# Kernel tuning notes

Hardware: AMD Instinct MI355X
Metric: run time of the kernel (lower is better)

## Reference

```python
import jax, jax.numpy as jnp
import numpy as np

PATCH = 16
TOP_K = 5
EPS = 1e-12


def l2_normalize(x, axis):
    sq = jnp.sum(x * x, axis=axis, keepdims=True)
    return x * jax.lax.rsqrt(jnp.maximum(sq, EPS))


def patch_embed(imgs, conv_w, conv_b):
    # imgs: (P, 3, 32, 32) -> (P, n_patches=4, D=768)
    y = jax.lax.conv_general_dilated(
        imgs, conv_w, window_strides=(PATCH, PATCH), padding='VALID',
        dimension_numbers=('NCHW', 'OIHW', 'NCHW'))  # (P, D, 2, 2)
    y = y + conv_b[None, :, None, None]
    P, D = y.shape[0], y.shape[1]
    return y.reshape(P, D, -1).transpose(0, 2, 1)  # (P, 4, D)


def setup_inputs() -> dict:
    key = jax.random.key(0)
    k1, k2, k3, k4 = jax.random.split(key, 4)
    B, N, D = 256, 196, 768
    P = 32  # pool_size
    x_embed = jax.random.normal(k1, (B, N, D), dtype=jnp.float32)
    # uniform(-1, 1) init as in the torch module
    prompt = jax.random.uniform(k2, (P, 3, 32, 32), dtype=jnp.float32, minval=-1.0, maxval=1.0)
    prompt_key = jax.random.uniform(k3, (P, D), dtype=jnp.float32, minval=-1.0, maxval=1.0)
    conv_w = jax.random.normal(k4, (D, 3, PATCH, PATCH), dtype=jnp.float32) * 0.02
    conv_b = jnp.zeros((D,), dtype=jnp.float32)
    return {'x_embed': x_embed, 'prompt': prompt, 'prompt_key': prompt_key,
            'conv_w': conv_w, 'conv_b': conv_b}


def reference(x_embed, prompt, prompt_key, conv_w, conv_b):
    B = x_embed.shape[0]
    prompt_embed = patch_embed(prompt, conv_w, conv_b)      # (P, 4, D)

    x_embed_mean = jnp.mean(x_embed, axis=1)                # (B, D), embedding_key='mean'
    prompt_norm = l2_normalize(prompt_key, axis=1)          # (P, D)
    x_embed_norm = l2_normalize(x_embed_mean, axis=1)       # (B, D)
    similarity = x_embed_norm @ prompt_norm.T               # (B, P)

    _, idx = jax.lax.top_k(similarity, TOP_K)               # (B, top_k)

    batched_prompt_embed = prompt_embed[idx]                # (B, top_k, 4, D)
    Bq, K, L, D = batched_prompt_embed.shape
    batched_prompt_embed = batched_prompt_embed.reshape(Bq, K * L, D)

    batched_key_norm = prompt_norm[idx]                     # (B, top_k, D)
    reduce_sim = jnp.sum(batched_key_norm * x_embed_norm[:, None, :]) / B

    prompted_embedding = jnp.concatenate([batched_prompt_embed, x_embed], axis=1)
    return prompted_embedding, reduce_sim, similarity, idx
```

## Files before the change

kernel.cpp:

```cpp
#include <hip/hip_runtime.h>

typedef unsigned short u16;
typedef unsigned int u32;

#define BB 256
#define NN 196
#define DD 768
#define PP 32
#define TOPK 5
#define NROW 216

#define OUT0_ELTS (BB * NROW * DD)
#define RS_OFF    OUT0_ELTS
#define SIM_OFF   (OUT0_ELTS + 1)
#define IDX_OFF   (OUT0_ELTS + 1 + BB * PP)

#define WS_PNORM  0
#define WS_PEMB   98304
#define WS_IDX    491520

__global__ __launch_bounds__(256) void k_prep(const float* __restrict__ pkey,
                                              const float* __restrict__ prompt,
                                              const float* __restrict__ cw,
                                              const float* __restrict__ cb,
                                              float* __restrict__ pnorm,
                                              float* __restrict__ pemb) {
    const int t = threadIdx.x;
    if (blockIdx.x < PP) {
        const int p = blockIdx.x;
        const float* row = pkey + (size_t)p * DD;
        float v0 = row[t], v1 = row[t + 256], v2 = row[t + 512];
        float sq = v0 * v0 + v1 * v1 + v2 * v2;
#pragma unroll
        for (int off = 32; off; off >>= 1) sq += __shfl_down(sq, off);
        __shared__ float wsum[4];
        __shared__ float rshared;
        if ((t & 63) == 0) wsum[t >> 6] = sq;
        __syncthreads();
        if (t == 0) rshared = rsqrtf(fmaxf(wsum[0] + wsum[1] + wsum[2] + wsum[3], 1e-12f));
        __syncthreads();
        float r = rshared;
        float* orow = pnorm + (size_t)p * DD;
        orow[t] = v0 * r;
        orow[t + 256] = v1 * r;
        orow[t + 512] = v2 * r;
    } else {
        const int bxx = blockIdx.x - PP;
        const int chunk = bxx / 32, pg = bxx - chunk * 32;
        const int m0 = pg * 4;
        const int n = chunk * 256 + t;
        __shared__ float patch[4 * DD];
        for (int idx = t; idx < 4 * DD; idx += 256) {
            const int j = idx / DD, kk = idx - j * DD;
            const int c = kk >> 8, rem = kk & 255;
            const int kh = rem >> 4, kw = rem & 15;
            const int m = m0 + j;
            const int p = m >> 2, l = m & 3;
            patch[idx] = prompt[(size_t)p * 3072 + (size_t)c * 1024
                                + ((l >> 1) * 16 + kh) * 32 + (l & 1) * 16 + kw];
        }
        __syncthreads();
        const float4* wrow = (const float4*)(cw + (size_t)n * DD);
        const float4* p0 = (const float4*)(patch);
        const float4* p1 = (const float4*)(patch + DD);
        const float4* p2 = (const float4*)(patch + 2 * DD);
        const float4* p3 = (const float4*)(patch + 3 * DD);
        float a0 = 0.f, a1 = 0.f, a2 = 0.f, a3 = 0.f;
#pragma unroll 4
        for (int kk = 0; kk < 192; ++kk) {
            const float4 w = wrow[kk];
            const float4 q0 = p0[kk], q1 = p1[kk], q2 = p2[kk], q3 = p3[kk];
            a0 += q0.x * w.x + q0.y * w.y + q0.z * w.z + q0.w * w.w;
            a1 += q1.x * w.x + q1.y * w.y + q1.z * w.z + q1.w * w.w;
            a2 += q2.x * w.x + q2.y * w.y + q2.z * w.z + q2.w * w.w;
            a3 += q3.x * w.x + q3.y * w.y + q3.z * w.z + q3.w * w.w;
        }
        const float bias = cb[n];
        pemb[(size_t)(m0 + 0) * DD + n] = a0 + bias;
        pemb[(size_t)(m0 + 1) * DD + n] = a1 + bias;
        pemb[(size_t)(m0 + 2) * DD + n] = a2 + bias;
        pemb[(size_t)(m0 + 3) * DD + n] = a3 + bias;
    }
}

__global__ __launch_bounds__(768) void k_fused(const float* __restrict__ x,
                                               const float* __restrict__ pnorm,
                                               const float* __restrict__ pemb,
                                               float* __restrict__ out,
                                               int* __restrict__ idx_ws) {
    const int b = blockIdx.x;
    const int t = threadIdx.x;
    const int g = t / 192, c = t - g * 192;
    const float* xb = x + (size_t)b * (NN * DD);
    float* ob = out + (size_t)b * (NROW * DD) + 20 * DD;
    float4 s = make_float4(0.f, 0.f, 0.f, 0.f);
#pragma unroll 7
    for (int i = 0; i < 49; ++i) {
        const int row = g + 4 * i;
        float4 v = *((const float4*)(xb + (size_t)row * DD) + c);
        s.x += v.x; s.y += v.y; s.z += v.z; s.w += v.w;
        *((float4*)(ob + (size_t)row * DD) + c) = v;
    }
    __shared__ float4 comb[768];
    __shared__ float xm[768];
    __shared__ float sims[PP];
    __shared__ float wred[12];
    __shared__ float rsh;
    __shared__ int lidx[TOPK];
    comb[g * 192 + c] = s;
    __syncthreads();
    if (g == 0) {
        float4 s0 = comb[c], s1 = comb[192 + c], s2 = comb[384 + c], s3 = comb[576 + c];
        const float inv = 1.0f / NN;
        xm[4 * c + 0] = (s0.x + s1.x + s2.x + s3.x) * inv;
        xm[4 * c + 1] = (s0.y + s1.y + s2.y + s3.y) * inv;
        xm[4 * c + 2] = (s0.z + s1.z + s2.z + s3.z) * inv;
        xm[4 * c + 3] = (s0.w + s1.w + s2.w + s3.w) * inv;
    }
    __syncthreads();
    float sq = xm[t] * xm[t];
#pragma unroll
    for (int off = 32; off; off >>= 1) sq += __shfl_down(sq, off);
    if ((t & 63) == 0) wred[t >> 6] = sq;
    __syncthreads();
    if (t == 0) {
        float tot = 0.f;
        for (int i = 0; i < 12; ++i) tot += wred[i];
        rsh = rsqrtf(fmaxf(tot, 1e-12f));
    }
    __syncthreads();
    const float r = rsh;
    if (t < 512) {
        const int p = t >> 4, sub = t & 15;
        const float* pr = pnorm + (size_t)p * DD;
        float acc = 0.f;
#pragma unroll 8
        for (int j = 0; j < 48; ++j) {
            const int k = sub + (j << 4);
            acc += xm[k] * pr[k];
        }
        acc += __shfl_down(acc, 8, 16);
        acc += __shfl_down(acc, 4, 16);
        acc += __shfl_down(acc, 2, 16);
        acc += __shfl_down(acc, 1, 16);
        if (sub == 0) {
            const float sv = acc * r;
            sims[p] = sv;
            out[SIM_OFF + b * PP + p] = sv;
        }
    }
    __syncthreads();
    if (t == 0) {
        unsigned used = 0;
        for (int k = 0; k < TOPK; ++k) {
            float best = -1e30f;
            int bi = 0;
            for (int q = 0; q < PP; ++q) {
                if (!((used >> q) & 1u) && sims[q] > best) { best = sims[q]; bi = q; }
            }
            used |= 1u << bi;
            lidx[k] = bi;
            idx_ws[b * TOPK + k] = bi;
            out[IDX_OFF + b * TOPK + k] = (float)bi;
        }
    }
    __syncthreads();
    float4* dst = (float4*)(out + (size_t)b * (NROW * DD));
    const float4* src = (const float4*)pemb;
    for (int v = t; v < 20 * 192; v += 768) {
        const int row = v / 192;
        const int off = v - row * 192;
        const int srow = lidx[row >> 2] * 4 + (row & 3);
        dst[row * 192 + off] = src[srow * 192 + off];
    }
}

__global__ __launch_bounds__(256) void k_final(const float* __restrict__ out_sim,
                                               const int* __restrict__ idx_ws,
                                               float* __restrict__ out_rs) {
    const int t = threadIdx.x;
    float s = 0.f;
#pragma unroll
    for (int k = 0; k < TOPK; ++k)
        s += out_sim[t * PP + idx_ws[t * TOPK + k]];
#pragma unroll
    for (int off = 32; off; off >>= 1) s += __shfl_down(s, off);
    __shared__ float wsum[4];
    if ((t & 63) == 0) wsum[t >> 6] = s;
    __syncthreads();
    if (t == 0) *out_rs = (wsum[0] + wsum[1] + wsum[2] + wsum[3]) * (1.0f / BB);
}

extern "C" void kernel_launch(void* const* d_in, const int* in_sizes, int n_in,
                              void* d_out, int out_size, void* d_ws, size_t ws_size,
                              hipStream_t stream) {
    const float* x      = (const float*)d_in[0];
    const float* prompt = (const float*)d_in[1];
    const float* pkey   = (const float*)d_in[2];
    const float* cw     = (const float*)d_in[3];
    const float* cb     = (const float*)d_in[4];
    float* out = (float*)d_out;
    char* ws = (char*)d_ws;

    float* pnorm = (float*)(ws + WS_PNORM);
    float* pemb  = (float*)(ws + WS_PEMB);
    int*   idxw  = (int*)(ws + WS_IDX);

    k_prep<<<PP + 96, 256, 0, stream>>>(pkey, prompt, cw, cb, pnorm, pemb);
    k_fused<<<BB, 768, 0, stream>>>(x, pnorm, pemb, out, idxw);
    k_final<<<1, 256, 0, stream>>>(out + SIM_OFF, idxw, out + RS_OFF);
}
```

Baseline: 343.7 us.

## Batch nontemporal x loads/stores and use wave-shuffle top-k selection

The copy-and-sum loop over x is restructured into groups of seven nontemporal loads issued before their stores, which raises memory-level parallelism and avoids cache pollution. The serial single-thread top-k over 32 similarities becomes a wave-wide shuffle argmax repeated five times. The prompt-embedding gather stores also become nontemporal. The cost is higher register pressure from holding seven float4 values per thread, plus a different tie-breaking order in the argmax.

```diff
diff --git a/kernel.cpp b/kernel.cpp
--- a/kernel.cpp
+++ b/kernel.cpp
@@ -2,6 +2,7 @@
 
 typedef unsigned short u16;
 typedef unsigned int u32;
+typedef float __attribute__((ext_vector_type(4))) f32x4;
 
 #define BB 256
 #define NN 196
@@ -93,15 +94,23 @@
     const int g = t / 192, c = t - g * 192;
     const float* xb = x + (size_t)b * (NN * DD);
     float* ob = out + (size_t)b * (NROW * DD) + 20 * DD;
-    float4 s = make_float4(0.f, 0.f, 0.f, 0.f);
-#pragma unroll 7
-    for (int i = 0; i < 49; ++i) {
-        const int row = g + 4 * i;
-        float4 v = *((const float4*)(xb + (size_t)row * DD) + c);
-        s.x += v.x; s.y += v.y; s.z += v.z; s.w += v.w;
-        *((float4*)(ob + (size_t)row * DD) + c) = v;
-    }
-    __shared__ float4 comb[768];
+    f32x4 s = (f32x4)(0.f);
+#pragma unroll
+    for (int o = 0; o < 7; ++o) {
+        f32x4 vv[7];
+#pragma unroll
+        for (int i = 0; i < 7; ++i) {
+            const int row = g + 4 * (o * 7 + i);
+            vv[i] = __builtin_nontemporal_load((const f32x4*)(xb + (size_t)row * DD) + c);
+        }
+#pragma unroll
+        for (int i = 0; i < 7; ++i) {
+            const int row = g + 4 * (o * 7 + i);
+            s += vv[i];
+            __builtin_nontemporal_store(vv[i], (f32x4*)(ob + (size_t)row * DD) + c);
+        }
+    }
+    __shared__ f32x4 comb[768];
     __shared__ float xm[768];
     __shared__ float sims[PP];
     __shared__ float wred[12];
@@ -110,12 +119,13 @@
     comb[g * 192 + c] = s;
     __syncthreads();
     if (g == 0) {
-        float4 s0 = comb[c], s1 = comb[192 + c], s2 = comb[384 + c], s3 = comb[576 + c];
+        f32x4 s0 = comb[c], s1 = comb[192 + c], s2 = comb[384 + c], s3 = comb[576 + c];
         const float inv = 1.0f / NN;
-        xm[4 * c + 0] = (s0.x + s1.x + s2.x + s3.x) * inv;
-        xm[4 * c + 1] = (s0.y + s1.y + s2.y + s3.y) * inv;
-        xm[4 * c + 2] = (s0.z + s1.z + s2.z + s3.z) * inv;
-        xm[4 * c + 3] = (s0.w + s1.w + s2.w + s3.w) * inv;
+        f32x4 m4 = (s0 + s1 + s2 + s3) * inv;
+        xm[4 * c + 0] = m4.x;
+        xm[4 * c + 1] = m4.y;
+        xm[4 * c + 2] = m4.z;
+        xm[4 * c + 3] = m4.w;
     }
     __syncthreads();
     float sq = xm[t] * xm[t];
@@ -150,28 +160,33 @@
         }
     }
     __syncthreads();
-    if (t == 0) {
-        unsigned used = 0;
+    if (t < 64) {
+        float v = (t < PP) ? sims[t] : -1e30f;
+#pragma unroll
         for (int k = 0; k < TOPK; ++k) {
-            float best = -1e30f;
-            int bi = 0;
-            for (int q = 0; q < PP; ++q) {
-                if (!((used >> q) & 1u) && sims[q] > best) { best = sims[q]; bi = q; }
+            float bv = v; int bbi = t;
+#pragma unroll
+            for (int off = 32; off; off >>= 1) {
+                const float ov = __shfl_xor(bv, off);
+                const int   oi = __shfl_xor(bbi, off);
+                if (ov > bv || (ov == bv && oi < bbi)) { bv = ov; bbi = oi; }
             }
-            used |= 1u << bi;
-            lidx[k] = bi;
-            idx_ws[b * TOPK + k] = bi;
-            out[IDX_OFF + b * TOPK + k] = (float)bi;
-        }
-    }
-    __syncthreads();
-    float4* dst = (float4*)(out + (size_t)b * (NROW * DD));
-    const float4* src = (const float4*)pemb;
+            if (t == 0) {
+                lidx[k] = bbi;
+                idx_ws[b * TOPK + k] = bbi;
+                out[IDX_OFF + b * TOPK + k] = (float)bbi;
+            }
+            if (t == bbi) v = -1e30f;
+        }
+    }
+    __syncthreads();
+    f32x4* dst = (f32x4*)(out + (size_t)b * (NROW * DD));
+    const f32x4* src = (const f32x4*)pemb;
     for (int v = t; v < 20 * 192; v += 768) {
         const int row = v / 192;
         const int off = v - row * 192;
         const int srow = lidx[row >> 2] * 4 + (row & 3);
-        dst[row * 192 + off] = src[srow * 192 + off];
+        __builtin_nontemporal_store(src[srow * 192 + off], dst + row * 192 + off);
     }
 }
 
```

Result: faster. 329.8 us (-4.1%).
